# Optimization experiments

Hardware: AMD Instinct MI355X
Metric: run time of the kernel (lower is better)

Reference implementation:

```python
import jax, jax.numpy as jnp
import numpy as np

WINDOW = 7
SHIFT = 3
NUM_HEADS = 12
DIM = 384
FFN = 4 * DIM
EPS = 1e-5


def _rel_pos_index(w):
    coords = np.stack(np.meshgrid(np.arange(w), np.arange(w), indexing='ij'))  # [2,w,w]
    flat = coords.reshape(2, -1)
    rel = (flat[:, :, None] - flat[:, None, :]).transpose(1, 2, 0)  # [w*w, w*w, 2]
    rel[..., 0] += w - 1
    rel[..., 1] += w - 1
    rel[..., 0] *= 2 * w - 1
    return rel.sum(-1).astype(np.int32)  # [w*w, w*w]


def _attn_mask(hp, wp, w, s):
    # replicate get_attn_mask: region labeling, window partition, pairwise diff
    img = np.zeros((hp, wp), dtype=np.float32)
    cnt = 0
    for hs in (slice(0, -w), slice(-w, -s), slice(-s, None)):
        for ws in (slice(0, -w), slice(-w, -s), slice(-s, None)):
            img[hs, ws] = cnt
            cnt += 1
    mw = img.reshape(hp // w, w, wp // w, w).transpose(0, 2, 1, 3).reshape(-1, w * w)
    diff = mw[:, None, :] - mw[:, :, None]  # unsqueeze(1) - unsqueeze(2)
    return jnp.asarray(np.where(diff != 0, -100.0, 0.0).astype(np.float32))


def _ln(x, g, b):
    mu = jnp.mean(x, -1, keepdims=True)
    var = jnp.mean(jnp.square(x - mu), -1, keepdims=True)
    return (x - mu) * jax.lax.rsqrt(var + EPS) * g + b


def setup_inputs() -> dict:
    key = jax.random.key(0)
    ks = jax.random.split(key, 12)
    B, H, W, C = 8, 56, 56, DIM
    sd = 0.02
    inp = {
        'hidden_states': jax.random.normal(ks[0], (B, H * W, C), jnp.float32),
        'ln1_g': jnp.ones((C,), jnp.float32), 'ln1_b': jnp.zeros((C,), jnp.float32),
        'q_w': jax.random.normal(ks[1], (C, C), jnp.float32) * sd, 'q_b': jnp.zeros((C,), jnp.float32),
        'k_w': jax.random.normal(ks[2], (C, C), jnp.float32) * sd, 'k_b': jnp.zeros((C,), jnp.float32),
        'v_w': jax.random.normal(ks[3], (C, C), jnp.float32) * sd, 'v_b': jnp.zeros((C,), jnp.float32),
        'rpb_table': jax.random.normal(ks[4], ((2 * WINDOW - 1) ** 2, NUM_HEADS), jnp.float32) * sd,
        'rp_index': jnp.asarray(_rel_pos_index(WINDOW)),
        'proj_w': jax.random.normal(ks[5], (C, C), jnp.float32) * sd, 'proj_b': jnp.zeros((C,), jnp.float32),
        'ln2_g': jnp.ones((C,), jnp.float32), 'ln2_b': jnp.zeros((C,), jnp.float32),
        'fc1_w': jax.random.normal(ks[6], (C, FFN), jnp.float32) * sd, 'fc1_b': jnp.zeros((FFN,), jnp.float32),
        'fc2_w': jax.random.normal(ks[7], (FFN, C), jnp.float32) * sd, 'fc2_b': jnp.zeros((C,), jnp.float32),
        'height': H, 'width': W,
    }
    return inp


def reference(hidden_states, ln1_g, ln1_b, q_w, q_b, k_w, k_b, v_w, v_b,
              rpb_table, rp_index, proj_w, proj_b, ln2_g, ln2_b,
              fc1_w, fc1_b, fc2_w, fc2_b, height, width):
    w, s, nh = WINDOW, SHIFT, NUM_HEADS
    B, L, C = hidden_states.shape
    hd = C // nh
    shortcut = hidden_states

    x = _ln(hidden_states, ln1_g, ln1_b).reshape(B, height, width, C)
    pad_b = (w - height % w) % w
    pad_r = (w - width % w) % w
    if pad_b or pad_r:
        x = jnp.pad(x, ((0, 0), (0, pad_b), (0, pad_r), (0, 0)))
    Hp, Wp = height + pad_b, width + pad_r

    if s > 0:
        x = jnp.roll(x, shift=(-s, -s), axis=(1, 2))

    # window partition -> [B*nW, w*w, C]
    N = w * w
    xw = x.reshape(B, Hp // w, w, Wp // w, w, C).transpose(0, 1, 3, 2, 4, 5).reshape(-1, N, C)

    q = (xw @ q_w + q_b).reshape(-1, N, nh, hd).transpose(0, 2, 1, 3)
    k = (xw @ k_w + k_b).reshape(-1, N, nh, hd).transpose(0, 2, 1, 3)
    v = (xw @ v_w + v_b).reshape(-1, N, nh, hd).transpose(0, 2, 1, 3)

    scores = jnp.einsum('whnd,whmd->whnm', q, k) / jnp.sqrt(jnp.float32(hd))
    bias = rpb_table[rp_index.reshape(-1)].reshape(N, N, nh).transpose(2, 0, 1)
    scores = scores + bias[None]

    if s > 0:
        mask = _attn_mask(Hp, Wp, w, s)  # [nW, N, N]
        nW = mask.shape[0]
        scores = scores.reshape(B, nW, nh, N, N) + mask[None, :, None]
        scores = scores.reshape(-1, nh, N, N)

    probs = jax.nn.softmax(scores, axis=-1)
    ctx = jnp.einsum('whnm,whmd->whnd', probs, v).transpose(0, 2, 1, 3).reshape(-1, N, C)
    attn_out = ctx @ proj_w + proj_b

    # window reverse
    xr = attn_out.reshape(B, Hp // w, Wp // w, w, w, C).transpose(0, 1, 3, 2, 4, 5).reshape(B, Hp, Wp, C)
    if s > 0:
        xr = jnp.roll(xr, shift=(s, s), axis=(1, 2))
    if pad_b or pad_r:
        xr = xr[:, :height, :width, :]
    xr = xr.reshape(B, height * width, C)

    h = shortcut + xr
    y = _ln(h, ln2_g, ln2_b)
    y = jax.nn.gelu(y @ fc1_w + fc1_b, approximate=False)
    return h + (y @ fc2_w + fc2_b)
```

## Files before the change

### kernel.cpp

```cpp
#include <hip/hip_runtime.h>
#include <hip/hip_bf16.h>

typedef unsigned short u16;
typedef short bf16x8 __attribute__((ext_vector_type(8)));
typedef float f32x4 __attribute__((ext_vector_type(4)));

__device__ __forceinline__ u16 f2bf(float x) {
  __hip_bfloat16 h = __float2bfloat16(x);
  return *reinterpret_cast<u16*>(&h);
}
__device__ __forceinline__ float bf2f(u16 x) {
  __hip_bfloat16 h = *reinterpret_cast<__hip_bfloat16*>(&x);
  return __bfloat162float(h);
}
__device__ __forceinline__ float rdany(const void* p, size_t i, int f) {
  return f ? ((const float*)p)[i] : bf2f(((const u16*)p)[i]);
}

__device__ __forceinline__ void gld_lds16(const u16* g, u16* l) {
  __builtin_amdgcn_global_load_lds(
      (const __attribute__((address_space(1))) void*)g,
      (__attribute__((address_space(3))) void*)l, 16, 0, 0);
}

__device__ __forceinline__ float gelu_fast(float x) {
  float z = fabsf(x) * 0.70710678118654752f;
  float t = 1.f / (1.f + 0.3275911f * z);
  float p = t * (0.254829592f +
            t * (-0.284496736f +
            t * (1.421413741f +
            t * (-1.453152027f + t * 1.061405429f))));
  float er = 1.f - p * __expf(-z * z);
  er = (x < 0.f) ? -er : er;
  return 0.5f * x * (1.f + er);
}

__global__ void detect_k(const u16* __restrict__ ln1g_raw, int* __restrict__ flag) {
  if (threadIdx.x == 0 && blockIdx.x == 0)
    *flag = (ln1g_raw[0] == 0 && ln1g_raw[2] == 0) ? 1 : 0;
}

__global__ __launch_bounds__(256) void prep_k(
    const void* qw, const void* kw, const void* vw, const void* pw,
    const void* f1w, const void* f2w,
    u16* __restrict__ qwT, u16* __restrict__ kwT, u16* __restrict__ vwT,
    u16* __restrict__ pwT, u16* __restrict__ f1T, u16* __restrict__ f2T,
    const void* s0, const void* s1, const void* s2, const void* s3,
    const void* s4, const void* s5, const void* s6, const void* s7,
    const void* s8, const void* s9, const void* s10,
    u16* __restrict__ vecdst, const int* __restrict__ flag) {
  int f = *flag;
  int b = blockIdx.x;
  if (b >= 1728) {
    const void* srcs[11] = {s0, s1, s2, s3, s4, s5, s6, s7, s8, s9, s10};
    const int offs[12] = {0, 384, 768, 1152, 1536, 1920, 2304, 2688, 3072, 3456, 4992, 7020};
    int tid = threadIdx.y * 32 + threadIdx.x;
    for (int i = tid; i < 7020; i += 256) {
      int seg = 0;
#pragma unroll
      for (int t = 1; t < 11; t++) seg += (i >= offs[t]) ? 1 : 0;
      vecdst[i] = f2bf(rdany(srcs[seg], i - offs[seg], f));
    }
    return;
  }
  const void* src; u16* dst; int R, C, bx, by;
  if (b < 576) {
    int m = b / 144, t = b - m * 144;
    src = (m == 0) ? qw : (m == 1) ? kw : (m == 2) ? vw : pw;
    dst = (m == 0) ? qwT : (m == 1) ? kwT : (m == 2) ? vwT : pwT;
    R = 384; C = 384; bx = t % 12; by = t / 12;
  } else if (b < 1152) {
    int t = b - 576; src = f1w; dst = f1T; R = 384; C = 1536;
    bx = t % 48; by = t / 48;
  } else {
    int t = b - 1152; src = f2w; dst = f2T; R = 1536; C = 384;
    bx = t % 12; by = t / 12;
  }
  __shared__ u16 tbuf[32][33];
  int x = threadIdx.x, y = threadIdx.y;
  int gx = bx * 32, gy = by * 32;
#pragma unroll
  for (int j = 0; j < 32; j += 8)
    tbuf[y + j][x] = f2bf(rdany(src, (size_t)(gy + y + j) * C + gx + x, f));
  __syncthreads();
#pragma unroll
  for (int j = 0; j < 32; j += 8) dst[(size_t)(gx + y + j) * R + gy + x] = tbuf[x][y + j];
}

__global__ __launch_bounds__(256) void ln1_window_k(
    const void* __restrict__ hid, const u16* __restrict__ g,
    const u16* __restrict__ b, u16* __restrict__ xw, int rowoff,
    const int* __restrict__ flag) {
  int f = *flag;
  int wv = threadIdx.x >> 6, lane = threadIdx.x & 63;
  int lrow = blockIdx.x * 4 + wv;
  int row = rowoff + lrow;
  int wid = row / 49, n = row - wid * 49;
  int bimg = wid >> 6, w8 = wid & 63;
  int wi = w8 >> 3, wj = w8 & 7;
  int p = n / 7, q = n - p * 7;
  int si = wi * 7 + p + 3; if (si >= 56) si -= 56;
  int sj = wj * 7 + q + 3; if (sj >= 56) sj -= 56;
  size_t src = ((size_t)bimg * 3136 + si * 56 + sj) * 384;
  float x[6]; float s = 0.f, s2 = 0.f;
#pragma unroll
  for (int e = 0; e < 6; e++) {
    x[e] = rdany(hid, src + e * 64 + lane, f);
    s += x[e]; s2 += x[e] * x[e];
  }
#pragma unroll
  for (int off = 32; off; off >>= 1) { s += __shfl_xor(s, off); s2 += __shfl_xor(s2, off); }
  float mu = s * (1.f / 384.f);
  float var = s2 * (1.f / 384.f) - mu * mu;
  float rs = 1.f / sqrtf(var + 1e-5f);
  size_t dst = (size_t)lrow * 384;
#pragma unroll
  for (int e = 0; e < 6; e++) {
    int c = e * 64 + lane;
    float yv = (x[e] - mu) * rs * bf2f(g[c]) + bf2f(b[c]);
    xw[dst + c] = f2bf(yv);
  }
}

__global__ __launch_bounds__(256) void ln2_k(
    const float* hsrc, const u16* __restrict__ g,
    const u16* __restrict__ b, u16* __restrict__ out) {
  int wv = threadIdx.x >> 6, lane = threadIdx.x & 63;
  int row = blockIdx.x * 4 + wv;
  size_t src = (size_t)row * 384;
  float x[6]; float s = 0.f, s2 = 0.f;
#pragma unroll
  for (int e = 0; e < 6; e++) {
    x[e] = hsrc[src + e * 64 + lane];
    s += x[e]; s2 += x[e] * x[e];
  }
#pragma unroll
  for (int off = 32; off; off >>= 1) { s += __shfl_xor(s, off); s2 += __shfl_xor(s2, off); }
  float mu = s * (1.f / 384.f);
  float var = s2 * (1.f / 384.f) - mu * mu;
  float rs = 1.f / sqrtf(var + 1e-5f);
#pragma unroll
  for (int e = 0; e < 6; e++) {
    int c = e * 64 + lane;
    float yv = (x[e] - mu) * rs * bf2f(g[c]) + bf2f(b[c]);
    out[src + c] = f2bf(yv);
  }
}

template <int EPI>
__global__ __launch_bounds__(256, 4) void gemm_bt(
    const u16* __restrict__ A, const u16* __restrict__ Bt,
    const u16* __restrict__ bias, void* outB,
    const void* __restrict__ shortcut, const float* hres,
    int M, int N, int K, int gmoff, int gx, const int* __restrict__ flag) {
  __shared__ __align__(16) u16 As[2][128 * 32];
  __shared__ __align__(16) u16 Bs[2][128 * 32];
  int bx = blockIdx.x;
  if (bx >= gx) return;
  int tid = threadIdx.x;
  int m0 = bx * 128, n0 = blockIdx.y * 128;
  int lane = tid & 63, wv = tid >> 6;
  int wm = (wv >> 1) * 64, wn = (wv & 1) * 64;
  int l15 = lane & 15, quad = lane >> 4;
  f32x4 acc[4][4];
#pragma unroll
  for (int a = 0; a < 4; a++)
#pragma unroll
    for (int c = 0; c < 4; c++) acc[a][c] = (f32x4){0.f, 0.f, 0.f, 0.f};

  int rowS[2], cS[2], wbS[2];
#pragma unroll
  for (int i = 0; i < 2; i++) {
    int id = i * 256 + tid;
    rowS[i] = id >> 2;
    cS[i] = id & 3;
    wbS[i] = (id & ~63) * 8;
  }

#define STAGE(buf, kb_)                                                       \
  {                                                                           \
    _Pragma("unroll") for (int i = 0; i < 2; i++) {                           \
      gld_lds16(A + (size_t)(m0 + rowS[i]) * K + (kb_) + cS[i] * 8,           \
                &As[buf][wbS[i]]);                                            \
      gld_lds16(Bt + (size_t)(n0 + rowS[i]) * K + (kb_) + cS[i] * 8,          \
                &Bs[buf][wbS[i]]);                                            \
    }                                                                         \
  }

  STAGE(0, 0);
  int cur = 0;
  for (int kb = 0; kb < K; kb += 32) {
    if (kb + 32 < K) {
      STAGE(cur ^ 1, kb + 32);
      asm volatile("s_waitcnt vmcnt(4)" ::: "memory");
    } else {
      asm volatile("s_waitcnt vmcnt(0)" ::: "memory");
    }
    __builtin_amdgcn_s_barrier();
    __builtin_amdgcn_sched_barrier(0);
    __builtin_amdgcn_s_setprio(1);
    {
      bf16x8 af[4], bfv[4];
#pragma unroll
      for (int mi = 0; mi < 4; mi++)
        af[mi] = *(const bf16x8*)&As[cur][(wm + mi * 16 + l15) * 32 + quad * 8];
#pragma unroll
      for (int ni = 0; ni < 4; ni++)
        bfv[ni] = *(const bf16x8*)&Bs[cur][(wn + ni * 16 + l15) * 32 + quad * 8];
#pragma unroll
      for (int mi = 0; mi < 4; mi++)
#pragma unroll
        for (int ni = 0; ni < 4; ni++)
          acc[mi][ni] = __builtin_amdgcn_mfma_f32_16x16x32_bf16(af[mi], bfv[ni], acc[mi][ni], 0, 0, 0);
    }
    __builtin_amdgcn_s_setprio(0);
    __builtin_amdgcn_sched_barrier(0);
    __builtin_amdgcn_s_barrier();
    cur ^= 1;
  }
#undef STAGE

  int f = (EPI == 2) ? *flag : 0;
  float biasv[4];
#pragma unroll
  for (int ni = 0; ni < 4; ni++) biasv[ni] = bf2f(bias[n0 + wn + ni * 16 + l15]);
  int seg = n0 / 384;
#pragma unroll
  for (int mi = 0; mi < 4; mi++) {
#pragma unroll
    for (int r = 0; r < 4; r++) {
      int gm = m0 + wm + mi * 16 + quad * 4 + r;
      size_t orow = 0;
      if (EPI == 2) {
        int grow = gmoff + gm;
        int wid = grow / 49, nIn = grow - wid * 49;
        int bimg = wid >> 6, w8 = wid & 63;
        int wi = w8 >> 3, wj = w8 & 7;
        int p = nIn / 7, q = nIn - p * 7;
        int oi = wi * 7 + p + 3; if (oi >= 56) oi -= 56;
        int oj = wj * 7 + q + 3; if (oj >= 56) oj -= 56;
        orow = ((size_t)bimg * 3136 + oi * 56 + oj) * 384;
      }
#pragma unroll
      for (int ni = 0; ni < 4; ni++) {
        int gn = n0 + wn + ni * 16 + l15;
        float v = acc[mi][ni][r] + biasv[ni];
        if (EPI == 1) {
          v = gelu_fast(v);
          ((u16*)outB)[(size_t)gm * N + gn] = f2bf(v);
        } else if (EPI == 2) {
          float hv = rdany(shortcut, orow + gn, f) + v;
          hv = fminf(fmaxf(hv, -1000.f), 1000.f);
          ((float*)outB)[orow + gn] = hv;
        } else if (EPI == 3) {
          float t = v + hres[(size_t)gm * N + gn];
          t = fminf(fmaxf(t, -1000.f), 1000.f);
          ((float*)outB)[(size_t)gm * N + gn] = t;
        } else {
          u16* dst = (u16*)outB + (size_t)seg * M * 384;
          dst[(size_t)gm * 384 + (gn - seg * 384)] = f2bf(v);
        }
      }
    }
  }
}

__global__ __launch_bounds__(256) void attn_k(
    const u16* __restrict__ Q, const u16* __restrict__ Kb, const u16* __restrict__ V,
    const u16* __restrict__ rpb, const int* __restrict__ rpi,
    u16* __restrict__ ctx, int wdoff) {
  __shared__ __align__(16) u16 qs[64 * 56];
  __shared__ __align__(16) u16 ks_[64 * 56];
  __shared__ __align__(16) u16 vt[32 * 72];
  __shared__ float S[64 * 65];
  __shared__ __align__(16) u16 P[64 * 72];
  __shared__ int regid[49];
  int lwd = blockIdx.x, hh = blockIdx.y;
  int wd = wdoff + lwd;
  int tid = threadIdx.x;
  int w8 = wd & 63, wi = w8 >> 3, wj = w8 & 7;

  for (int idx = tid; idx < 840; idx += 256) {
    int rr = idx / 56, cc = idx - rr * 56;
    qs[(49 + rr) * 56 + cc] = 0;
    ks_[(49 + rr) * 56 + cc] = 0;
  }
  for (int idx = tid; idx < 4608; idx += 256) P[idx] = 0;
  for (int idx = tid; idx < 480; idx += 256) {
    int d = idx / 15, m = 49 + (idx - d * 15);
    vt[d * 72 + m] = 0;
  }
  if (tid < 49) {
    int p = tid / 7, q = tid - p * 7;
    int rr = (wi == 7) ? (p < 4 ? 1 : 2) : 0;
    int cc = (wj == 7) ? (q < 4 ? 1 : 2) : 0;
    regid[tid] = rr * 3 + cc;
  }
  size_t base = ((size_t)lwd * 49) * 384 + hh * 32;
  for (int idx = tid; idx < 392; idx += 256) {
    int mat = idx >= 196;
    int rid = idx - mat * 196;
    int n = rid >> 2, c = rid & 3;
    uint4 val = *(const uint4*)((mat ? Kb : Q) + base + (size_t)n * 384 + c * 8);
    *(uint4*)&((mat ? ks_ : qs)[n * 56 + c * 8]) = val;
  }
  for (int idx = tid; idx < 196; idx += 256) {
    int n = idx >> 2, c = idx & 3;
    uint4 val = *(const uint4*)(V + base + (size_t)n * 384 + c * 8);
    u16 tmp[8];
    *(uint4*)tmp = val;
#pragma unroll
    for (int t = 0; t < 8; t++) vt[(c * 8 + t) * 72 + n] = tmp[t];
  }
  __syncthreads();

  int lane = tid & 63, wv = tid >> 6, l15 = lane & 15, quad = lane >> 4;
  f32x4 zero = (f32x4){0.f, 0.f, 0.f, 0.f};
  bf16x8 aq = *(const bf16x8*)&qs[(wv * 16 + l15) * 56 + quad * 8];
  f32x4 sc[4];
#pragma unroll
  for (int mi = 0; mi < 4; mi++) {
    bf16x8 bk = *(const bf16x8*)&ks_[(mi * 16 + l15) * 56 + quad * 8];
    sc[mi] = __builtin_amdgcn_mfma_f32_16x16x32_bf16(aq, bk, zero, 0, 0, 0);
  }
  const float scale = 0.17677669529663687f;
#pragma unroll
  for (int mi = 0; mi < 4; mi++) {
#pragma unroll
    for (int r = 0; r < 4; r++) {
      int n = wv * 16 + quad * 4 + r;
      int m = mi * 16 + l15;
      float v = sc[mi][r] * scale;
      if (n < 49 && m < 49) {
        v += bf2f(rpb[rpi[n * 49 + m] * 12 + hh]);
        if (regid[n] != regid[m]) v -= 100.f;
      }
      S[n * 65 + m] = v;
    }
  }
  __syncthreads();

  if (tid < 49) {
    float mx = -1e30f;
    for (int m = 0; m < 49; m++) {
      float sv = fminf(fmaxf(S[tid * 65 + m], -1e4f), 1e4f);
      S[tid * 65 + m] = sv;
      mx = fmaxf(mx, sv);
    }
    float sum = 0.f;
    for (int m = 0; m < 49; m++) {
      float e = expf(S[tid * 65 + m] - mx);
      sum += e;
      S[tid * 65 + m] = e;
    }
    float inv = 1.f / sum;
    for (int m = 0; m < 49; m++) P[tid * 72 + m] = f2bf(S[tid * 65 + m] * inv);
  }
  __syncthreads();

  f32x4 oacc[2]; oacc[0] = zero; oacc[1] = zero;
#pragma unroll
  for (int ks = 0; ks < 2; ks++) {
    bf16x8 ap = *(const bf16x8*)&P[(wv * 16 + l15) * 72 + ks * 32 + quad * 8];
#pragma unroll
    for (int ni = 0; ni < 2; ni++) {
      bf16x8 bv = *(const bf16x8*)&vt[(ni * 16 + l15) * 72 + ks * 32 + quad * 8];
      oacc[ni] = __builtin_amdgcn_mfma_f32_16x16x32_bf16(ap, bv, oacc[ni], 0, 0, 0);
    }
  }
#pragma unroll
  for (int ni = 0; ni < 2; ni++) {
#pragma unroll
    for (int r = 0; r < 4; r++) {
      int n = wv * 16 + quad * 4 + r;
      if (n < 49) {
        int d = ni * 16 + l15;
        ctx[base + (size_t)n * 384 + d] = f2bf(oacc[ni][r]);
      }
    }
  }
}

static inline int pad8(int gx) { return (gx + 7) & ~7; }

extern "C" void kernel_launch(void* const* d_in, const int* in_sizes, int n_in,
                              void* d_out, int out_size, void* d_ws, size_t ws_size,
                              hipStream_t stream) {
  const void* hid = d_in[0];
  const void* ln1g = d_in[1];
  const void* ln1b = d_in[2];
  const void* qw = d_in[3];
  const void* qb = d_in[4];
  const void* kw = d_in[5];
  const void* kbias = d_in[6];
  const void* vw = d_in[7];
  const void* vb = d_in[8];
  const void* rpb = d_in[9];
  const int* rpi = (const int*)d_in[10];
  const void* pw = d_in[11];
  const void* pb = d_in[12];
  const void* ln2g = d_in[13];
  const void* ln2b = d_in[14];
  const void* f1w = d_in[15];
  const void* f1b = d_in[16];
  const void* f2w = d_in[17];
  const void* f2b = d_in[18];

  char* ws = (char*)d_ws;
  u16* wT = (u16*)ws;
  u16* qwT = wT;
  u16* kwT = qwT + 147456;
  u16* vwT = kwT + 147456;
  u16* pwT = vwT + 147456;
  u16* f1T = pwT + 147456;
  u16* f2T = f1T + 589824;
  u16* VEC = (u16*)(ws + 3538944);
  u16* s_ln1g = VEC + 0;
  u16* s_ln1b = VEC + 384;
  u16* s_qkvb = VEC + 768;
  u16* s_pb = VEC + 1920;
  u16* s_ln2g = VEC + 2304;
  u16* s_ln2b = VEC + 2688;
  u16* s_f2b = VEC + 3072;
  u16* s_f1b = VEC + 3456;
  u16* s_rpb = VEC + 4992;
  int* flag = (int*)(ws + 3552984);
  const size_t head = 3553280;

  size_t avail = (ws_size > head) ? ws_size - head : 0;
  int rows1 = (avail >= (size_t)25088 * 3072) ? 25088
            : (avail >= (size_t)12544 * 3072) ? 12544 : 6272;
  int rows2 = (avail >= (size_t)25088 * 3840) ? 25088
            : (avail >= (size_t)12544 * 3840) ? 12544 : 3584;

  u16* P1 = (u16*)(ws + head);
  u16* xw = P1;
  u16* Qb = P1 + (size_t)rows1 * 384;
  u16* Kb = Qb + (size_t)rows1 * 384;
  u16* Vb = Kb + (size_t)rows1 * 384;
  u16* y2 = P1;
  u16* f1o = P1 + (size_t)rows2 * 384;
  float* hbuf = (float*)d_out;

  detect_k<<<1, 64, 0, stream>>>((const u16*)ln1g, flag);
  dim3 tb(32, 8);
  prep_k<<<1729, tb, 0, stream>>>(qw, kw, vw, pw, f1w, f2w,
                                  qwT, kwT, vwT, pwT, f1T, f2T,
                                  ln1g, ln1b, qb, kbias, vb, pb, ln2g, ln2b,
                                  f2b, f1b, rpb, VEC, flag);

  for (int off = 0; off < 25088; off += rows1) {
    int gx = rows1 / 128;
    ln1_window_k<<<rows1 / 4, 256, 0, stream>>>(hid, s_ln1g, s_ln1b, xw, off, flag);
    gemm_bt<4><<<dim3(pad8(gx), 9), 256, 0, stream>>>(
        xw, qwT, s_qkvb, Qb, nullptr, nullptr, rows1, 1152, 384, 0, gx, flag);
    attn_k<<<dim3(rows1 / 49, 12), 256, 0, stream>>>(Qb, Kb, Vb, s_rpb, rpi, xw, off / 49);
    gemm_bt<2><<<dim3(pad8(gx), 3), 256, 0, stream>>>(
        xw, pwT, s_pb, hbuf, hid, nullptr, rows1, 384, 384, off, gx, flag);
  }

  for (int off = 0; off < 25088; off += rows2) {
    int gx = rows2 / 128;
    ln2_k<<<rows2 / 4, 256, 0, stream>>>(hbuf + (size_t)off * 384, s_ln2g, s_ln2b, y2);
    gemm_bt<1><<<dim3(pad8(gx), 12), 256, 0, stream>>>(
        y2, f1T, s_f1b, f1o, nullptr, nullptr, rows2, 1536, 384, 0, gx, flag);
    gemm_bt<3><<<dim3(pad8(gx), 3), 256, 0, stream>>>(
        f1o, f2T, s_f2b, hbuf + (size_t)off * 384, nullptr,
        hbuf + (size_t)off * 384, rows2, 384, 1536, 0, gx, flag);
  }
}
```

Measured before the change: 420.4 us.

## Parallelize attention softmax in registers and precompute gathered bias table

Replaces the 49-thread serial softmax over a shared-memory score buffer with per-wave register softmax using lane shuffles, removing the S buffer and two block barriers. Relative-position bias is gathered once per head into a contiguous table in the prep kernel, so the attention kernel no longer does a double-indirect lookup. Launch bounds are raised to encourage more resident blocks. The change relies on wave-local LDS ordering for P and drops the score clamp.

```diff
diff --git a/kernel.cpp b/kernel.cpp
--- a/kernel.cpp
+++ b/kernel.cpp
@@ -48,13 +48,21 @@
     const void* s0, const void* s1, const void* s2, const void* s3,
     const void* s4, const void* s5, const void* s6, const void* s7,
     const void* s8, const void* s9, const void* s10,
-    u16* __restrict__ vecdst, const int* __restrict__ flag) {
+    u16* __restrict__ vecdst, const int* __restrict__ rpi,
+    u16* __restrict__ biasT, const int* __restrict__ flag) {
   int f = *flag;
   int b = blockIdx.x;
   if (b >= 1728) {
+    int tid = threadIdx.y * 32 + threadIdx.x;
+    if (b == 1729) {
+      for (int i = tid; i < 28812; i += 256) {
+        int hh = i / 2401, r = i - hh * 2401;
+        biasT[i] = f2bf(rdany(s10, (size_t)rpi[r] * 12 + hh, f));
+      }
+      return;
+    }
     const void* srcs[11] = {s0, s1, s2, s3, s4, s5, s6, s7, s8, s9, s10};
     const int offs[12] = {0, 384, 768, 1152, 1536, 1920, 2304, 2688, 3072, 3456, 4992, 7020};
-    int tid = threadIdx.y * 32 + threadIdx.x;
     for (int i = tid; i < 7020; i += 256) {
       int seg = 0;
 #pragma unroll
@@ -265,14 +273,12 @@
   }
 }
 
-__global__ __launch_bounds__(256) void attn_k(
+__global__ __launch_bounds__(256, 5) void attn_k(
     const u16* __restrict__ Q, const u16* __restrict__ Kb, const u16* __restrict__ V,
-    const u16* __restrict__ rpb, const int* __restrict__ rpi,
-    u16* __restrict__ ctx, int wdoff) {
+    const u16* __restrict__ biasT, u16* __restrict__ ctx, int wdoff) {
   __shared__ __align__(16) u16 qs[64 * 56];
   __shared__ __align__(16) u16 ks_[64 * 56];
   __shared__ __align__(16) u16 vt[32 * 72];
-  __shared__ float S[64 * 65];
   __shared__ __align__(16) u16 P[64 * 72];
   __shared__ int regid[49];
   int lwd = blockIdx.x, hh = blockIdx.y;
@@ -285,7 +291,6 @@
     qs[(49 + rr) * 56 + cc] = 0;
     ks_[(49 + rr) * 56 + cc] = 0;
   }
-  for (int idx = tid; idx < 4608; idx += 256) P[idx] = 0;
   for (int idx = tid; idx < 480; idx += 256) {
     int d = idx / 15, m = 49 + (idx - d * 15);
     vt[d * 72 + m] = 0;
@@ -324,39 +329,46 @@
     sc[mi] = __builtin_amdgcn_mfma_f32_16x16x32_bf16(aq, bk, zero, 0, 0, 0);
   }
   const float scale = 0.17677669529663687f;
+
+  int rm[4];
 #pragma unroll
   for (int mi = 0; mi < 4; mi++) {
-#pragma unroll
-    for (int r = 0; r < 4; r++) {
-      int n = wv * 16 + quad * 4 + r;
+    int m = mi * 16 + l15;
+    rm[mi] = (m < 49) ? regid[m] : -2;
+  }
+  float pv[4][4];
+#pragma unroll
+  for (int r = 0; r < 4; r++) {
+    int n = wv * 16 + quad * 4 + r;
+    int rn = (n < 49) ? regid[n] : -1;
+    const u16* brow = biasT + hh * 2401 + n * 49;
+#pragma unroll
+    for (int mi = 0; mi < 4; mi++) {
       int m = mi * 16 + l15;
       float v = sc[mi][r] * scale;
       if (n < 49 && m < 49) {
-        v += bf2f(rpb[rpi[n * 49 + m] * 12 + hh]);
-        if (regid[n] != regid[m]) v -= 100.f;
+        v += bf2f(brow[m]);
+        if (rn != rm[mi]) v -= 100.f;
       }
-      S[n * 65 + m] = v;
-    }
-  }
-  __syncthreads();
-
-  if (tid < 49) {
-    float mx = -1e30f;
-    for (int m = 0; m < 49; m++) {
-      float sv = fminf(fmaxf(S[tid * 65 + m], -1e4f), 1e4f);
-      S[tid * 65 + m] = sv;
-      mx = fmaxf(mx, sv);
-    }
+      if (m >= 49) v = -1e4f;
+      pv[r][mi] = v;
+    }
+    float mx = fmaxf(fmaxf(pv[r][0], pv[r][1]), fmaxf(pv[r][2], pv[r][3]));
+#pragma unroll
+    for (int off = 1; off < 16; off <<= 1) mx = fmaxf(mx, __shfl_xor(mx, off));
     float sum = 0.f;
-    for (int m = 0; m < 49; m++) {
-      float e = expf(S[tid * 65 + m] - mx);
-      sum += e;
-      S[tid * 65 + m] = e;
-    }
+#pragma unroll
+    for (int mi = 0; mi < 4; mi++) {
+      pv[r][mi] = __expf(pv[r][mi] - mx);
+      sum += pv[r][mi];
+    }
+#pragma unroll
+    for (int off = 1; off < 16; off <<= 1) sum += __shfl_xor(sum, off);
     float inv = 1.f / sum;
-    for (int m = 0; m < 49; m++) P[tid * 72 + m] = f2bf(S[tid * 65 + m] * inv);
-  }
-  __syncthreads();
+#pragma unroll
+    for (int mi = 0; mi < 4; mi++)
+      P[n * 72 + mi * 16 + l15] = f2bf(pv[r][mi] * inv);
+  }
 
   f32x4 oacc[2]; oacc[0] = zero; oacc[1] = zero;
 #pragma unroll
@@ -425,7 +437,8 @@
   u16* s_f1b = VEC + 3456;
   u16* s_rpb = VEC + 4992;
   int* flag = (int*)(ws + 3552984);
-  const size_t head = 3553280;
+  u16* biasT = (u16*)(ws + 3552992);
+  const size_t head = 3610624;
 
   size_t avail = (ws_size > head) ? ws_size - head : 0;
   int rows1 = (avail >= (size_t)25088 * 3072) ? 25088
@@ -444,17 +457,17 @@
 
   detect_k<<<1, 64, 0, stream>>>((const u16*)ln1g, flag);
   dim3 tb(32, 8);
-  prep_k<<<1729, tb, 0, stream>>>(qw, kw, vw, pw, f1w, f2w,
+  prep_k<<<1730, tb, 0, stream>>>(qw, kw, vw, pw, f1w, f2w,
                                   qwT, kwT, vwT, pwT, f1T, f2T,
                                   ln1g, ln1b, qb, kbias, vb, pb, ln2g, ln2b,
-                                  f2b, f1b, rpb, VEC, flag);
+                                  f2b, f1b, rpb, VEC, rpi, biasT, flag);
 
   for (int off = 0; off < 25088; off += rows1) {
     int gx = rows1 / 128;
     ln1_window_k<<<rows1 / 4, 256, 0, stream>>>(hid, s_ln1g, s_ln1b, xw, off, flag);
     gemm_bt<4><<<dim3(pad8(gx), 9), 256, 0, stream>>>(
         xw, qwT, s_qkvb, Qb, nullptr, nullptr, rows1, 1152, 384, 0, gx, flag);
-    attn_k<<<dim3(rows1 / 49, 12), 256, 0, stream>>>(Qb, Kb, Vb, s_rpb, rpi, xw, off / 49);
+    attn_k<<<dim3(rows1 / 49, 12), 256, 0, stream>>>(Qb, Kb, Vb, biasT, xw, off / 49);
     gemm_bt<2><<<dim3(pad8(gx), 3), 256, 0, stream>>>(
         xw, pwT, s_pb, hbuf, hid, nullptr, rows1, 384, 384, off, gx, flag);
   }
```

New measurement: 401.5 us. 4.5% less time.
